# Performance work log

Hardware: AMD Instinct MI355X
Metric: run time of the kernel (lower is better)

## Reference

```python
import jax, jax.numpy as jnp
import numpy as np

RES = 128            # occupancy grid resolution per axis
HIDDEN = 128         # MLP width
PE_POS = 10          # positional-encoding freqs for xyz
PE_DIR = 4           # positional-encoding freqs for viewdirs
S_MAX = 192          # max marching steps per ray
STEP = 0.027         # render_step_size (~aabb diagonal / S_MAX)
ERT = 1e-4           # early_stop_eps (transmittance threshold)
AABB_MIN = -1.5
AABB_MAX = 1.5
WHITE_BKGD = 1.0     # white_bkgd=True


def _posenc(x, L):
    # x: [..., 3] -> [..., 3 + 6L]
    freqs = 2.0 ** jnp.arange(L, dtype=x.dtype)
    xb = x[..., None, :] * freqs[:, None]                 # [..., L, 3]
    enc = jnp.concatenate([jnp.sin(xb), jnp.cos(xb)], axis=-1)  # [..., L, 6]
    return jnp.concatenate([x, enc.reshape(x.shape[:-1] + (-1,))], axis=-1)


def setup_inputs() -> dict:
    key = jax.random.key(0)
    ks = jax.random.split(key, 8)
    B, N = 1, 2048
    # camera origins on a sphere of radius 2.5 outside the aabb, rays aimed near the center
    o = jax.random.normal(ks[0], (B, N, 3), dtype=jnp.float32)
    o = o / jnp.linalg.norm(o, axis=-1, keepdims=True) * 2.5
    target = jax.random.normal(ks[1], (B, N, 3), dtype=jnp.float32) * 0.3
    d = target - o
    d = d / jnp.linalg.norm(d, axis=-1, keepdims=True)
    occ_grid = jax.random.bernoulli(ks[2], 0.3, (RES, RES, RES))
    din_pos = 3 + 6 * PE_POS   # 63
    din_dir = 3 + 6 * PE_DIR   # 27
    sc = lambda n: 1.0 / np.sqrt(n)
    W0 = jax.random.normal(ks[3], (din_pos, HIDDEN), dtype=jnp.float32) * sc(din_pos)
    W1 = jax.random.normal(ks[4], (HIDDEN, HIDDEN), dtype=jnp.float32) * sc(HIDDEN)
    w_sigma = jax.random.normal(ks[5], (HIDDEN, 1), dtype=jnp.float32) * sc(HIDDEN)
    W2 = jax.random.normal(ks[6], (HIDDEN + din_dir, HIDDEN), dtype=jnp.float32) * sc(HIDDEN)
    w_rgb = jax.random.normal(ks[7], (HIDDEN, 3), dtype=jnp.float32) * sc(HIDDEN)
    return {"rays_o": o, "viewdirs": d, "occ_grid": occ_grid,
            "W0": W0, "W1": W1, "w_sigma": w_sigma, "W2": W2, "w_rgb": w_rgb}


def reference(rays_o, viewdirs, occ_grid, W0, W1, w_sigma, W2, w_rgb):
    B, N, _ = rays_o.shape
    o = rays_o.reshape(-1, 3)          # [R, 3]
    d = viewdirs.reshape(-1, 3)        # [R, 3]
    R = o.shape[0]
    # ray / aabb intersection
    inv_d = 1.0 / jnp.where(jnp.abs(d) < 1e-9, 1e-9, d)
    t0 = (AABB_MIN - o) * inv_d
    t1 = (AABB_MAX - o) * inv_d
    t_near = jnp.maximum(jnp.max(jnp.minimum(t0, t1), axis=-1), 0.0)  # [R]
    t_far = jnp.min(jnp.maximum(t0, t1), axis=-1)                     # [R]
    # fixed-step marching (padded to S_MAX, masked) == nerfacc sampling with occ grid
    i = jnp.arange(S_MAX, dtype=rays_o.dtype)
    t_start = t_near[:, None] + STEP * i[None, :]   # [R, S]
    t_end = t_start + STEP
    t_mid = t_start + 0.5 * STEP
    inside = (t_mid < t_far[:, None]) & ((t_far > t_near)[:, None])
    pts = o[:, None, :] + d[:, None, :] * t_mid[..., None]  # [R, S, 3]
    # occupancy lookup (skip empty cells)
    gidx = jnp.clip(((pts - AABB_MIN) / (AABB_MAX - AABB_MIN) * RES).astype(jnp.int32), 0, RES - 1)
    occ = occ_grid[gidx[..., 0], gidx[..., 1], gidx[..., 2]]  # [R, S] bool
    mask = inside & occ
    # NeRF MLP (rgb_alpha_fn): sigma from pos, rgb from pos feature + viewdir
    pe_p = _posenc(pts.reshape(-1, 3), PE_POS)                               # [RS, 63]
    pe_d = _posenc(jnp.broadcast_to(d[:, None, :], pts.shape).reshape(-1, 3), PE_DIR)  # [RS, 27]
    h = jax.nn.relu(pe_p @ W0)
    h = jax.nn.relu(h @ W1)
    sigma = (h @ w_sigma).reshape(R, S_MAX)
    h2 = jax.nn.relu(jnp.concatenate([h, pe_d], axis=-1) @ W2)
    rgb = jax.nn.sigmoid(h2 @ w_rgb).reshape(R, S_MAX, 3)
    # alpha compositing (nerfacc.rendering) with early termination
    delta = t_end - t_start
    alpha = (1.0 - jnp.exp(-jax.nn.relu(sigma) * delta)) * mask.astype(sigma.dtype)
    trans = jnp.cumprod(1.0 - alpha + 1e-10, axis=-1)
    T = jnp.concatenate([jnp.ones((R, 1), alpha.dtype), trans[:, :-1]], axis=-1)  # exclusive
    T = T * (T > ERT).astype(T.dtype)  # early ray termination
    w = T * alpha                      # [R, S]
    rgb_map = jnp.einsum('rs,rsc->rc', w, rgb)
    opacity = jnp.sum(w, axis=-1, keepdims=True)
    depth = jnp.sum(w * t_mid, axis=-1, keepdims=True)
    rgb_map = rgb_map + (1.0 - opacity) * WHITE_BKGD
    return (rgb_map.reshape(B, N, 3), depth.reshape(B, N, 1), opacity.reshape(B, N, 1))
```

## Files before the change

kernel.cpp:

```cpp
#include <hip/hip_runtime.h>
#include <stdint.h>

#define NRAYS 2048
#define SMAX  192
#define RESG  128
#define STEPF 0.027f
#define ERTF  1e-4f
#define CAP   (NRAYS * SMAX)

typedef __attribute__((ext_vector_type(8)))  short bf16x8;
typedef __attribute__((ext_vector_type(16))) float f32x16;

__device__ __forceinline__ uint32_t f2b(float x) {
    uint32_t u = __builtin_bit_cast(uint32_t, x);
    return (u + 0x7fffu + ((u >> 16) & 1u)) >> 16;
}
__device__ __forceinline__ uint32_t bpack(float lo, float hi) {
    return f2b(lo) | (f2b(hi) << 16);
}

__device__ __forceinline__ void ray_aabb(float ox, float oy, float oz,
                                         float dx, float dy, float dz,
                                         float& tn, float& tf) {
    float ix = 1.0f / ((fabsf(dx) < 1e-9f) ? 1e-9f : dx);
    float iy = 1.0f / ((fabsf(dy) < 1e-9f) ? 1e-9f : dy);
    float iz = 1.0f / ((fabsf(dz) < 1e-9f) ? 1e-9f : dz);
    float t0x = (-1.5f - ox) * ix, t1x = (1.5f - ox) * ix;
    float t0y = (-1.5f - oy) * iy, t1y = (1.5f - oy) * iy;
    float t0z = (-1.5f - oz) * iz, t1z = (1.5f - oz) * iz;
    float tnx = fminf(t0x, t1x), tfx = fmaxf(t0x, t1x);
    float tny = fminf(t0y, t1y), tfy = fmaxf(t0y, t1y);
    float tnz = fminf(t0z, t1z), tfz = fmaxf(t0z, t1z);
    tn = fmaxf(fmaxf(fmaxf(tnx, tny), tnz), 0.0f);
    tf = fminf(fminf(tfx, tfy), tfz);
}

__global__ __launch_bounds__(256) void k_count_prep(
        const float* __restrict__ ro, const float* __restrict__ rd,
        const int* __restrict__ occ,
        const float* __restrict__ W0, const float* __restrict__ W1,
        const float* __restrict__ W2,
        int* __restrict__ rayCount, unsigned long long* __restrict__ masks,
        uint32_t* __restrict__ wfrag) {
    int b = blockIdx.x;
    if (b >= NRAYS / 4) {
        int pb = b - NRAYS / 4;
        int lane = threadIdx.x;
        if (lane >= 64) return;
        int g = pb >> 2, oc = pb & 3;
        int out = oc * 32 + (lane & 31);
        const float* W; int kbase, Klim;
        if (g < 4)       { W = W0; kbase = g * 16;        Klim = 63;  }
        else if (g < 12) { W = W1; kbase = (g - 4) * 16;  Klim = 128; }
        else             { W = W2; kbase = (g - 12) * 16; Klim = 155; }
        uint32_t d[4];
        #pragma unroll
        for (int h = 0; h < 4; ++h) {
            int k0 = kbase + ((lane >> 5) << 3) + h * 2;
            float lo = (k0     < Klim) ? W[(size_t)k0 * 128 + out]       : 0.0f;
            float hi = (k0 + 1 < Klim) ? W[(size_t)(k0 + 1) * 128 + out] : 0.0f;
            d[h] = bpack(lo, hi);
        }
        ((uint4*)wfrag)[pb * 64 + lane] = make_uint4(d[0], d[1], d[2], d[3]);
        return;
    }
    int r = b * 4 + (threadIdx.x >> 6);
    int lane = threadIdx.x & 63;
    float ox = ro[r*3+0], oy = ro[r*3+1], oz = ro[r*3+2];
    float dx = rd[r*3+0], dy = rd[r*3+1], dz = rd[r*3+2];
    float tn, tf;
    ray_aabb(ox, oy, oz, dx, dy, dz, tn, tf);
    int cnt = 0;
    #pragma unroll
    for (int c = 0; c < 3; ++c) {
        int s = c * 64 + lane;
        float t_mid = (tn + STEPF * (float)s) + 0.5f * STEPF;
        bool inside = (t_mid < tf) && (tf > tn);
        bool act = false;
        if (inside) {
            float px = ox + dx * t_mid;
            float py = oy + dy * t_mid;
            float pz = oz + dz * t_mid;
            int gx = min(max((int)((px + 1.5f) / 3.0f * 128.0f), 0), RESG - 1);
            int gy = min(max((int)((py + 1.5f) / 3.0f * 128.0f), 0), RESG - 1);
            int gz = min(max((int)((pz + 1.5f) / 3.0f * 128.0f), 0), RESG - 1);
            act = occ[(gx * RESG + gy) * RESG + gz] != 0;
        }
        unsigned long long mb = __ballot(act);
        if (lane == 0) masks[r * 3 + c] = mb;
        cnt += __popcll(mb);
    }
    if (lane == 0) rayCount[r] = cnt;
}

__global__ __launch_bounds__(1024) void k_scan(
        const int* __restrict__ rayCount, int* __restrict__ rayOff,
        int* __restrict__ cnt_total) {
    __shared__ int wsum[16];
    int tid = threadIdx.x;
    int a = rayCount[2 * tid], b = rayCount[2 * tid + 1];
    int s = a + b;
    int lane = tid & 63, w = tid >> 6;
    int v = s;
    #pragma unroll
    for (int off = 1; off < 64; off <<= 1) {
        int t = __shfl_up(v, off);
        if (lane >= off) v += t;
    }
    if (lane == 63) wsum[w] = v;
    __syncthreads();
    if (tid < 16) {
        int x = wsum[tid];
        #pragma unroll
        for (int off = 1; off < 16; off <<= 1) {
            int t = __shfl_up(x, off, 16);
            if (tid >= off) x += t;
        }
        wsum[tid] = x;
    }
    __syncthreads();
    int wbase = (w == 0) ? 0 : wsum[w - 1];
    int incl = wbase + v;
    int excl = incl - s;
    rayOff[2 * tid]     = excl;
    rayOff[2 * tid + 1] = excl + a;
    if (tid == 1023) cnt_total[0] = incl;
}

__global__ __launch_bounds__(256) void k_fill(
        const float* __restrict__ ro, const float* __restrict__ rd,
        const int* __restrict__ rayOff, const unsigned long long* __restrict__ masks,
        int* __restrict__ rayid, float4* __restrict__ pos) {
    int r = blockIdx.x * 4 + (threadIdx.x >> 6);
    int lane = threadIdx.x & 63;
    float ox = ro[r*3+0], oy = ro[r*3+1], oz = ro[r*3+2];
    float dx = rd[r*3+0], dy = rd[r*3+1], dz = rd[r*3+2];
    float tn, tf;
    ray_aabb(ox, oy, oz, dx, dy, dz, tn, tf);
    int base = rayOff[r];
    #pragma unroll
    for (int c = 0; c < 3; ++c) {
        unsigned long long m = masks[r * 3 + c];
        if ((m >> lane) & 1ull) {
            int within = __popcll(m & ((1ull << lane) - 1ull));
            int s = c * 64 + lane;
            float t_mid = (tn + STEPF * (float)s) + 0.5f * STEPF;
            float px = ox + dx * t_mid;
            float py = oy + dy * t_mid;
            float pz = oz + dz * t_mid;
            rayid[base + within] = r;
            pos[base + within] = make_float4(px, py, pz, t_mid);
        }
        base += __popcll(m);
    }
}

__global__ __launch_bounds__(512) void k_mlp(
        const uint32_t* __restrict__ wfrag, const float* __restrict__ wsig,
        const float* __restrict__ wrgb, const float* __restrict__ vd,
        const int* __restrict__ cnt, const int* __restrict__ rayid,
        const float4* __restrict__ pos, float4* __restrict__ rgba) {
    __shared__ __align__(16) short actA[128 * 128];
    __shared__ __align__(16) short bufB[128 * 256];
    __shared__ float4 sPos[128];
    __shared__ int    sRay[128];
    __shared__ float  sV[128];
    __shared__ float  sR[384];

    const int tid  = threadIdx.x;
    const int wave = tid >> 6;
    const int lane = tid & 63;
    const int oc   = wave & 3;
    const int sc   = wave >> 2;
    const int lo5  = lane & 31;
    const int hi5  = lane >> 5;

    if (tid < 128) sV[tid] = wsig[tid];
    if (tid >= 128 && tid < 512) sR[tid - 128] = wrgb[tid - 128];

    bf16x8 wf[22];
    {
        const uint4* src = (const uint4*)wfrag;
        #pragma unroll
        for (int g = 0; g < 22; ++g) {
            uint4 v = src[(g * 4 + oc) * 64 + lane];
            wf[g] = __builtin_bit_cast(bf16x8, v);
        }
    }

    const int total  = *cnt;
    const int ntiles = (total + 127) >> 7;
    const int mrow   = sc * 64 + lo5;
    const int rswz   = (mrow & 15) << 4;

    for (int t = blockIdx.x; t < ntiles; t += gridDim.x) {
        const int base = t << 7;
        __syncthreads();
        if (tid < 128) {
            int gi = base + tid;
            if (gi < total) { sRay[tid] = rayid[gi]; sPos[tid] = pos[gi]; }
            else            { sRay[tid] = 0; sPos[tid] = make_float4(0.f,0.f,0.f,0.f); }
        }
        __syncthreads();

        {
            int m = tid >> 2, p = tid & 3;
            float4 P = sPos[m];
            int swz = (m & 15) << 4;
            #pragma unroll
            for (int half = 0; half < 2; ++half) {
                uint32_t dw[4];
                #pragma unroll
                for (int jp = 0; jp < 4; ++jp) {
                    float v[2];
                    #pragma unroll
                    for (int q = 0; q < 2; ++q) {
                        int c = p * 16 + half * 8 + jp * 2 + q;
                        float val;
                        if (c < 3)        val = (c == 0) ? P.x : ((c == 1) ? P.y : P.z);
                        else if (c >= 63) val = 0.0f;
                        else {
                            int cc = c - 3, l = cc / 6, jj = cc - 6 * l;
                            int a3 = (jj >= 3) ? jj - 3 : jj;
                            float comp = (a3 == 0) ? P.x : ((a3 == 1) ? P.y : P.z);
                            float arg = comp * (float)(1 << l);
                            val = (jj < 3) ? __sinf(arg) : __cosf(arg);
                        }
                        v[q] = val;
                    }
                    dw[jp] = bpack(v[0], v[1]);
                }
                *(uint4*)((char*)actA + m * 256 + ((p * 32 + half * 16) ^ swz)) = make_uint4(dw[0], dw[1], dw[2], dw[3]);
            }
            {
                int ray = sRay[m];
                float Dx = vd[ray*3+0], Dy = vd[ray*3+1], Dz = vd[ray*3+2];
                uint32_t dw[4];
                #pragma unroll
                for (int jp = 0; jp < 4; ++jp) {
                    float v[2];
                    #pragma unroll
                    for (int q = 0; q < 2; ++q) {
                        int c = p * 8 + jp * 2 + q;
                        float val;
                        if (c < 3)        val = (c == 0) ? Dx : ((c == 1) ? Dy : Dz);
                        else if (c >= 27) val = 0.0f;
                        else {
                            int cc = c - 3, l = cc / 6, jj = cc - 6 * l;
                            int a3 = (jj >= 3) ? jj - 3 : jj;
                            float comp = (a3 == 0) ? Dx : ((a3 == 1) ? Dy : Dz);
                            float arg = comp * (float)(1 << l);
                            val = (jj < 3) ? __sinf(arg) : __cosf(arg);
                        }
                        v[q] = val;
                    }
                    dw[jp] = bpack(v[0], v[1]);
                }
                *(uint4*)((char*)bufB + m * 512 + ((256 + p * 16) ^ swz)) = make_uint4(dw[0], dw[1], dw[2], dw[3]);
            }
        }
        __syncthreads();

        {
            f32x16 a0 = {}, a1 = {};
            #pragma unroll
            for (int kb = 0; kb < 4; ++kb) {
                int cb = (kb * 32 + (hi5 << 4)) ^ rswz;
                bf16x8 b0 = *(const bf16x8*)((const char*)actA + mrow * 256 + cb);
                bf16x8 b1 = *(const bf16x8*)((const char*)actA + (mrow + 32) * 256 + cb);
                a0 = __builtin_amdgcn_mfma_f32_32x32x16_bf16(wf[kb], b0, a0, 0, 0, 0);
                a1 = __builtin_amdgcn_mfma_f32_32x32x16_bf16(wf[kb], b1, a1, 0, 0, 0);
            }
            #pragma unroll
            for (int g = 0; g < 4; ++g) {
                int outb = (oc * 32 + g * 8 + (hi5 << 2)) * 2;
                *(uint2*)((char*)bufB + mrow * 512 + (outb ^ rswz)) =
                    make_uint2(bpack(fmaxf(a0[g*4+0],0.f), fmaxf(a0[g*4+1],0.f)),
                               bpack(fmaxf(a0[g*4+2],0.f), fmaxf(a0[g*4+3],0.f)));
                *(uint2*)((char*)bufB + (mrow + 32) * 512 + (outb ^ rswz)) =
                    make_uint2(bpack(fmaxf(a1[g*4+0],0.f), fmaxf(a1[g*4+1],0.f)),
                               bpack(fmaxf(a1[g*4+2],0.f), fmaxf(a1[g*4+3],0.f)));
            }
        }
        __syncthreads();

        {
            f32x16 a0 = {}, a1 = {};
            #pragma unroll
            for (int kb = 0; kb < 8; ++kb) {
                int cb = (kb * 32 + (hi5 << 4)) ^ rswz;
                bf16x8 b0 = *(const bf16x8*)((const char*)bufB + mrow * 512 + cb);
                bf16x8 b1 = *(const bf16x8*)((const char*)bufB + (mrow + 32) * 512 + cb);
                a0 = __builtin_amdgcn_mfma_f32_32x32x16_bf16(wf[4 + kb], b0, a0, 0, 0, 0);
                a1 = __builtin_amdgcn_mfma_f32_32x32x16_bf16(wf[4 + kb], b1, a1, 0, 0, 0);
            }
            #pragma unroll
            for (int g = 0; g < 4; ++g) {
                int outb = (oc * 32 + g * 8 + (hi5 << 2)) * 2;
                *(uint2*)((char*)actA + mrow * 256 + (outb ^ rswz)) =
                    make_uint2(bpack(fmaxf(a0[g*4+0],0.f), fmaxf(a0[g*4+1],0.f)),
                               bpack(fmaxf(a0[g*4+2],0.f), fmaxf(a0[g*4+3],0.f)));
                *(uint2*)((char*)actA + (mrow + 32) * 256 + (outb ^ rswz)) =
                    make_uint2(bpack(fmaxf(a1[g*4+0],0.f), fmaxf(a1[g*4+1],0.f)),
                               bpack(fmaxf(a1[g*4+2],0.f), fmaxf(a1[g*4+3],0.f)));
            }
        }
        __syncthreads();

        {
            f32x16 a0 = {}, a1 = {};
            #pragma unroll
            for (int kb = 0; kb < 8; ++kb) {
                int cb = (kb * 32 + (hi5 << 4)) ^ rswz;
                bf16x8 b0 = *(const bf16x8*)((const char*)actA + mrow * 256 + cb);
                bf16x8 b1 = *(const bf16x8*)((const char*)actA + (mrow + 32) * 256 + cb);
                a0 = __builtin_amdgcn_mfma_f32_32x32x16_bf16(wf[12 + kb], b0, a0, 0, 0, 0);
                a1 = __builtin_amdgcn_mfma_f32_32x32x16_bf16(wf[12 + kb], b1, a1, 0, 0, 0);
            }
            #pragma unroll
            for (int kb = 8; kb < 10; ++kb) {
                int cb = (kb * 32 + (hi5 << 4)) ^ rswz;
                bf16x8 b0 = *(const bf16x8*)((const char*)bufB + mrow * 512 + cb);
                bf16x8 b1 = *(const bf16x8*)((const char*)bufB + (mrow + 32) * 512 + cb);
                a0 = __builtin_amdgcn_mfma_f32_32x32x16_bf16(wf[12 + kb], b0, a0, 0, 0, 0);
                a1 = __builtin_amdgcn_mfma_f32_32x32x16_bf16(wf[12 + kb], b1, a1, 0, 0, 0);
            }
            #pragma unroll
            for (int g = 0; g < 4; ++g) {
                int outb = (oc * 32 + g * 8 + (hi5 << 2)) * 2;
                *(uint2*)((char*)bufB + mrow * 512 + (outb ^ rswz)) =
                    make_uint2(bpack(fmaxf(a0[g*4+0],0.f), fmaxf(a0[g*4+1],0.f)),
                               bpack(fmaxf(a0[g*4+2],0.f), fmaxf(a0[g*4+3],0.f)));
                *(uint2*)((char*)bufB + (mrow + 32) * 512 + (outb ^ rswz)) =
                    make_uint2(bpack(fmaxf(a1[g*4+0],0.f), fmaxf(a1[g*4+1],0.f)),
                               bpack(fmaxf(a1[g*4+2],0.f), fmaxf(a1[g*4+3],0.f)));
            }
        }
        __syncthreads();

        {
            int m = tid >> 2, p = tid & 3;
            int swz = (m & 15) << 4;
            float sp = 0.f, r0 = 0.f, r1 = 0.f, r2 = 0.f;
            #pragma unroll
            for (int hh = 0; hh < 4; ++hh) {
                uint4 q = *(const uint4*)((const char*)actA + m * 256 + ((p * 64 + hh * 16) ^ swz));
                uint32_t w[4] = {q.x, q.y, q.z, q.w};
                #pragma unroll
                for (int e = 0; e < 4; ++e) {
                    int j = p * 32 + hh * 8 + e * 2;
                    float a0 = __builtin_bit_cast(float, w[e] << 16);
                    float a1 = __builtin_bit_cast(float, w[e] & 0xffff0000u);
                    sp = fmaf(a0, sV[j], sp);
                    sp = fmaf(a1, sV[j + 1], sp);
                }
            }
            #pragma unroll
            for (int hh = 0; hh < 4; ++hh) {
                uint4 q = *(const uint4*)((const char*)bufB + m * 512 + ((p * 64 + hh * 16) ^ swz));
                uint32_t w[4] = {q.x, q.y, q.z, q.w};
                #pragma unroll
                for (int e = 0; e < 4; ++e) {
                    int j = p * 32 + hh * 8 + e * 2;
                    float a0 = __builtin_bit_cast(float, w[e] << 16);
                    float a1 = __builtin_bit_cast(float, w[e] & 0xffff0000u);
                    r0 = fmaf(a0, sR[j*3+0], r0); r1 = fmaf(a0, sR[j*3+1], r1); r2 = fmaf(a0, sR[j*3+2], r2);
                    r0 = fmaf(a1, sR[(j+1)*3+0], r0); r1 = fmaf(a1, sR[(j+1)*3+1], r1); r2 = fmaf(a1, sR[(j+1)*3+2], r2);
                }
            }
            #pragma unroll
            for (int off = 1; off < 4; off <<= 1) {
                sp += __shfl_xor(sp, off);
                r0 += __shfl_xor(r0, off);
                r1 += __shfl_xor(r1, off);
                r2 += __shfl_xor(r2, off);
            }
            if (p == 0 && (base + m) < total) {
                float alpha = 1.0f - __expf(-fmaxf(sp, 0.0f) * STEPF);
                float c0 = 1.0f / (1.0f + __expf(-r0));
                float c1 = 1.0f / (1.0f + __expf(-r1));
                float c2 = 1.0f / (1.0f + __expf(-r2));
                rgba[base + m] = make_float4(c0, c1, c2, alpha);
            }
        }
    }
}

__global__ __launch_bounds__(256) void k_render(
        const int* __restrict__ rayOff, const int* __restrict__ rayCount,
        const float4* __restrict__ rgba, const float* __restrict__ posw,
        float* __restrict__ out) {
    int r = blockIdx.x * 4 + (threadIdx.x >> 6);
    int lane = threadIdx.x & 63;
    int off = rayOff[r], cnt = rayCount[r];
    float T_run = 1.0f;
    float cr = 0.f, cg = 0.f, cb = 0.f, opa = 0.f, dep = 0.f;
    for (int j = 0; j < cnt; j += 64) {
        int idx = j + lane;
        float4 f = make_float4(0.f, 0.f, 0.f, 0.f);
        float tmid = 0.f;
        if (idx < cnt) {
            f = rgba[off + idx];
            tmid = posw[(size_t)(off + idx) * 4 + 3];
        }
        float p = (1.0f - f.w) + 1e-10f;
        #pragma unroll
        for (int o = 1; o < 64; o <<= 1) {
            float v = __shfl_up(p, o);
            if (lane >= o) p *= v;
        }
        float pprev = __shfl_up(p, 1);
        float Texc = (lane == 0) ? T_run : T_run * pprev;
        Texc = (Texc > ERTF) ? Texc : 0.0f;
        float w = Texc * f.w;
        cr += w * f.x; cg += w * f.y; cb += w * f.z;
        opa += w; dep += w * tmid;
        T_run *= __shfl(p, 63);
        if (T_run <= ERTF) break;
    }
    #pragma unroll
    for (int o = 32; o; o >>= 1) {
        cr  += __shfl_xor(cr, o);
        cg  += __shfl_xor(cg, o);
        cb  += __shfl_xor(cb, o);
        opa += __shfl_xor(opa, o);
        dep += __shfl_xor(dep, o);
    }
    if (lane == 0) {
        out[r * 3 + 0] = cr + (1.0f - opa);
        out[r * 3 + 1] = cg + (1.0f - opa);
        out[r * 3 + 2] = cb + (1.0f - opa);
        out[NRAYS * 3 + r] = dep;
        out[NRAYS * 4 + r] = opa;
    }
}

extern "C" void kernel_launch(void* const* d_in, const int* in_sizes, int n_in,
                              void* d_out, int out_size, void* d_ws, size_t ws_size,
                              hipStream_t stream) {
    const float* ro   = (const float*)d_in[0];
    const float* rd   = (const float*)d_in[1];
    const int*   occ  = (const int*)d_in[2];
    const float* W0   = (const float*)d_in[3];
    const float* W1   = (const float*)d_in[4];
    const float* wsig = (const float*)d_in[5];
    const float* W2   = (const float*)d_in[6];
    const float* wrgb = (const float*)d_in[7];
    float* out = (float*)d_out;

    char* ws = (char*)d_ws;
    int*                cnt_total = (int*)ws;
    int*                rayCount  = (int*)(ws + 16);
    int*                rayOff    = (int*)(ws + 8208);
    unsigned long long* masks     = (unsigned long long*)(ws + 16400);
    int*                rayid     = (int*)(ws + 65552);
    float4*             pos       = (float4*)(ws + 65552 + (size_t)CAP * 8);
    float4*             rgba      = (float4*)(ws + 65552 + (size_t)CAP * 24);
    uint32_t*           wfrag     = (uint32_t*)(ws + 65552 + (size_t)CAP * 40);

    k_count_prep <<<NRAYS / 4 + 88, 256, 0, stream>>>(ro, rd, occ, W0, W1, W2,
                                                      rayCount, masks, wfrag);
    k_scan  <<<1, 1024, 0, stream>>>(rayCount, rayOff, cnt_total);
    k_fill  <<<NRAYS / 4, 256, 0, stream>>>(ro, rd, rayOff, masks, rayid, pos);
    k_mlp   <<<256, 512, 0, stream>>>(wfrag, wsig, wrgb, rd, cnt_total, rayid, pos, rgba);
    k_render<<<NRAYS / 4, 256, 0, stream>>>(rayOff, rayCount, rgba, (const float*)pos, out);
}
```

Measured before the change: 114.2 us.

## Fuse count, scan, fill, MLP and render into one per-8-ray kernel

New measurement: 115.6 us. Within noise of the previous version (+1.2%).

```diff
diff --git a/kernel.cpp b/kernel.cpp
--- a/kernel.cpp
+++ b/kernel.cpp
@@ -6,7 +6,6 @@
 #define RESG  128
 #define STEPF 0.027f
 #define ERTF  1e-4f
-#define CAP   (NRAYS * SMAX)
 
 typedef __attribute__((ext_vector_type(8)))  short bf16x8;
 typedef __attribute__((ext_vector_type(16))) float f32x16;
@@ -35,42 +34,62 @@
     tf = fminf(fminf(tfx, tfy), tfz);
 }
 
-__global__ __launch_bounds__(256) void k_count_prep(
+__global__ __launch_bounds__(512) void k_fused(
         const float* __restrict__ ro, const float* __restrict__ rd,
         const int* __restrict__ occ,
         const float* __restrict__ W0, const float* __restrict__ W1,
-        const float* __restrict__ W2,
-        int* __restrict__ rayCount, unsigned long long* __restrict__ masks,
-        uint32_t* __restrict__ wfrag) {
-    int b = blockIdx.x;
-    if (b >= NRAYS / 4) {
-        int pb = b - NRAYS / 4;
-        int lane = threadIdx.x;
-        if (lane >= 64) return;
-        int g = pb >> 2, oc = pb & 3;
-        int out = oc * 32 + (lane & 31);
-        const float* W; int kbase, Klim;
-        if (g < 4)       { W = W0; kbase = g * 16;        Klim = 63;  }
-        else if (g < 12) { W = W1; kbase = (g - 4) * 16;  Klim = 128; }
-        else             { W = W2; kbase = (g - 12) * 16; Klim = 155; }
-        uint32_t d[4];
+        const float* __restrict__ wsig, const float* __restrict__ W2,
+        const float* __restrict__ wrgb, float* __restrict__ out) {
+    __shared__ __align__(16) short actA[128 * 128];
+    __shared__ __align__(16) short bufB[128 * 256];
+    __shared__ float4 rgbaL[8 * SMAX];
+    __shared__ unsigned short sList[8 * SMAX];
+    __shared__ float  sPD[8][28];
+    __shared__ float  sRD[8][8];
+    __shared__ float  sV[128];
+    __shared__ float  sR[384];
+    __shared__ int    sCnt[8];
+
+    const int tid  = threadIdx.x;
+    const int wave = tid >> 6;
+    const int lane = tid & 63;
+    const int oc   = wave & 3;
+    const int sc   = wave >> 2;
+    const int lo5  = lane & 31;
+    const int hi5  = lane >> 5;
+
+    if (tid < 128) sV[tid] = wsig[tid];
+    if (tid >= 128 && tid < 512) sR[tid - 128] = wrgb[tid - 128];
+
+    bf16x8 wf[22];
+    {
+        const int outc = oc * 32 + lo5;
         #pragma unroll
-        for (int h = 0; h < 4; ++h) {
-            int k0 = kbase + ((lane >> 5) << 3) + h * 2;
-            float lo = (k0     < Klim) ? W[(size_t)k0 * 128 + out]       : 0.0f;
-            float hi = (k0 + 1 < Klim) ? W[(size_t)(k0 + 1) * 128 + out] : 0.0f;
-            d[h] = bpack(lo, hi);
-        }
-        ((uint4*)wfrag)[pb * 64 + lane] = make_uint4(d[0], d[1], d[2], d[3]);
-        return;
-    }
-    int r = b * 4 + (threadIdx.x >> 6);
-    int lane = threadIdx.x & 63;
-    float ox = ro[r*3+0], oy = ro[r*3+1], oz = ro[r*3+2];
-    float dx = rd[r*3+0], dy = rd[r*3+1], dz = rd[r*3+2];
+        for (int g = 0; g < 22; ++g) {
+            const float* W; int kbase, Klim;
+            if (g < 4)       { W = W0; kbase = g * 16;        Klim = 63;  }
+            else if (g < 12) { W = W1; kbase = (g - 4) * 16;  Klim = 128; }
+            else             { W = W2; kbase = (g - 12) * 16; Klim = 155; }
+            uint32_t d[4];
+            #pragma unroll
+            for (int h = 0; h < 4; ++h) {
+                int k0 = kbase + (hi5 << 3) + h * 2;
+                float lo = (k0     < Klim) ? W[(size_t)k0 * 128 + outc]       : 0.0f;
+                float hi = (k0 + 1 < Klim) ? W[(size_t)(k0 + 1) * 128 + outc] : 0.0f;
+                d[h] = bpack(lo, hi);
+            }
+            uint4 v = make_uint4(d[0], d[1], d[2], d[3]);
+            wf[g] = __builtin_bit_cast(bf16x8, v);
+        }
+    }
+
+    const int r = blockIdx.x * 8 + wave;
+    const float ox = ro[r*3+0], oy = ro[r*3+1], oz = ro[r*3+2];
+    const float dx = rd[r*3+0], dy = rd[r*3+1], dz = rd[r*3+2];
     float tn, tf;
     ray_aabb(ox, oy, oz, dx, dy, dz, tn, tf);
-    int cnt = 0;
+    unsigned long long msk[3];
+    int myCnt = 0;
     #pragma unroll
     for (int c = 0; c < 3; ++c) {
         int s = c * 64 + lane;
@@ -87,125 +106,73 @@
             act = occ[(gx * RESG + gy) * RESG + gz] != 0;
         }
         unsigned long long mb = __ballot(act);
-        if (lane == 0) masks[r * 3 + c] = mb;
-        cnt += __popcll(mb);
-    }
-    if (lane == 0) rayCount[r] = cnt;
-}
-
-__global__ __launch_bounds__(1024) void k_scan(
-        const int* __restrict__ rayCount, int* __restrict__ rayOff,
-        int* __restrict__ cnt_total) {
-    __shared__ int wsum[16];
-    int tid = threadIdx.x;
-    int a = rayCount[2 * tid], b = rayCount[2 * tid + 1];
-    int s = a + b;
-    int lane = tid & 63, w = tid >> 6;
-    int v = s;
+        msk[c] = mb;
+        myCnt += __popcll(mb);
+    }
+    if (lane == 0) {
+        sCnt[wave] = myCnt;
+        sRD[wave][0] = ox; sRD[wave][1] = oy; sRD[wave][2] = oz;
+        sRD[wave][3] = dx; sRD[wave][4] = dy; sRD[wave][5] = dz;
+        sRD[wave][6] = tn;
+    }
+    if (lane < 28) {
+        float val = 0.0f;
+        if (lane < 3) val = (lane == 0) ? dx : ((lane == 1) ? dy : dz);
+        else if (lane < 27) {
+            int cc = lane - 3, l = cc / 6, jj = cc - 6 * l;
+            int a3 = (jj >= 3) ? jj - 3 : jj;
+            float comp = (a3 == 0) ? dx : ((a3 == 1) ? dy : dz);
+            float arg = comp * (float)(1 << l);
+            val = (jj < 3) ? __sinf(arg) : __cosf(arg);
+        }
+        sPD[wave][lane] = val;
+    }
+    __syncthreads();
+
+    int myBase = 0, total = 0;
     #pragma unroll
-    for (int off = 1; off < 64; off <<= 1) {
-        int t = __shfl_up(v, off);
-        if (lane >= off) v += t;
-    }
-    if (lane == 63) wsum[w] = v;
+    for (int i = 0; i < 8; ++i) {
+        int ci = sCnt[i];
+        if (i < wave) myBase += ci;
+        total += ci;
+    }
+    {
+        int run = myBase;
+        #pragma unroll
+        for (int c = 0; c < 3; ++c) {
+            unsigned long long mb = msk[c];
+            if ((mb >> lane) & 1ull) {
+                int within = __popcll(mb & ((1ull << lane) - 1ull));
+                sList[run + within] = (unsigned short)((wave << 8) | (c * 64 + lane));
+            }
+            run += __popcll(mb);
+        }
+    }
     __syncthreads();
-    if (tid < 16) {
-        int x = wsum[tid];
-        #pragma unroll
-        for (int off = 1; off < 16; off <<= 1) {
-            int t = __shfl_up(x, off, 16);
-            if (tid >= off) x += t;
-        }
-        wsum[tid] = x;
-    }
-    __syncthreads();
-    int wbase = (w == 0) ? 0 : wsum[w - 1];
-    int incl = wbase + v;
-    int excl = incl - s;
-    rayOff[2 * tid]     = excl;
-    rayOff[2 * tid + 1] = excl + a;
-    if (tid == 1023) cnt_total[0] = incl;
-}
-
-__global__ __launch_bounds__(256) void k_fill(
-        const float* __restrict__ ro, const float* __restrict__ rd,
-        const int* __restrict__ rayOff, const unsigned long long* __restrict__ masks,
-        int* __restrict__ rayid, float4* __restrict__ pos) {
-    int r = blockIdx.x * 4 + (threadIdx.x >> 6);
-    int lane = threadIdx.x & 63;
-    float ox = ro[r*3+0], oy = ro[r*3+1], oz = ro[r*3+2];
-    float dx = rd[r*3+0], dy = rd[r*3+1], dz = rd[r*3+2];
-    float tn, tf;
-    ray_aabb(ox, oy, oz, dx, dy, dz, tn, tf);
-    int base = rayOff[r];
-    #pragma unroll
-    for (int c = 0; c < 3; ++c) {
-        unsigned long long m = masks[r * 3 + c];
-        if ((m >> lane) & 1ull) {
-            int within = __popcll(m & ((1ull << lane) - 1ull));
-            int s = c * 64 + lane;
-            float t_mid = (tn + STEPF * (float)s) + 0.5f * STEPF;
-            float px = ox + dx * t_mid;
-            float py = oy + dy * t_mid;
-            float pz = oz + dz * t_mid;
-            rayid[base + within] = r;
-            pos[base + within] = make_float4(px, py, pz, t_mid);
-        }
-        base += __popcll(m);
-    }
-}
-
-__global__ __launch_bounds__(512) void k_mlp(
-        const uint32_t* __restrict__ wfrag, const float* __restrict__ wsig,
-        const float* __restrict__ wrgb, const float* __restrict__ vd,
-        const int* __restrict__ cnt, const int* __restrict__ rayid,
-        const float4* __restrict__ pos, float4* __restrict__ rgba) {
-    __shared__ __align__(16) short actA[128 * 128];
-    __shared__ __align__(16) short bufB[128 * 256];
-    __shared__ float4 sPos[128];
-    __shared__ int    sRay[128];
-    __shared__ float  sV[128];
-    __shared__ float  sR[384];
-
-    const int tid  = threadIdx.x;
-    const int wave = tid >> 6;
-    const int lane = tid & 63;
-    const int oc   = wave & 3;
-    const int sc   = wave >> 2;
-    const int lo5  = lane & 31;
-    const int hi5  = lane >> 5;
-
-    if (tid < 128) sV[tid] = wsig[tid];
-    if (tid >= 128 && tid < 512) sR[tid - 128] = wrgb[tid - 128];
-
-    bf16x8 wf[22];
-    {
-        const uint4* src = (const uint4*)wfrag;
-        #pragma unroll
-        for (int g = 0; g < 22; ++g) {
-            uint4 v = src[(g * 4 + oc) * 64 + lane];
-            wf[g] = __builtin_bit_cast(bf16x8, v);
-        }
-    }
-
-    const int total  = *cnt;
+
     const int ntiles = (total + 127) >> 7;
     const int mrow   = sc * 64 + lo5;
     const int rswz   = (mrow & 15) << 4;
 
-    for (int t = blockIdx.x; t < ntiles; t += gridDim.x) {
+    for (int t = 0; t < ntiles; ++t) {
         const int base = t << 7;
         __syncthreads();
-        if (tid < 128) {
-            int gi = base + tid;
-            if (gi < total) { sRay[tid] = rayid[gi]; sPos[tid] = pos[gi]; }
-            else            { sRay[tid] = 0; sPos[tid] = make_float4(0.f,0.f,0.f,0.f); }
-        }
-        __syncthreads();
 
         {
             int m = tid >> 2, p = tid & 3;
-            float4 P = sPos[m];
+            int gi = base + m;
+            float px = 0.f, py = 0.f, pz = 0.f;
+            int we = 0;
+            if (gi < total) {
+                int e = sList[gi];
+                we = e >> 8;
+                int s = e & 255;
+                float tnw = sRD[we][6];
+                float t_mid = (tnw + STEPF * (float)s) + 0.5f * STEPF;
+                px = sRD[we][0] + sRD[we][3] * t_mid;
+                py = sRD[we][1] + sRD[we][4] * t_mid;
+                pz = sRD[we][2] + sRD[we][5] * t_mid;
+            }
             int swz = (m & 15) << 4;
             #pragma unroll
             for (int half = 0; half < 2; ++half) {
@@ -217,12 +184,12 @@
                     for (int q = 0; q < 2; ++q) {
                         int c = p * 16 + half * 8 + jp * 2 + q;
                         float val;
-                        if (c < 3)        val = (c == 0) ? P.x : ((c == 1) ? P.y : P.z);
+                        if (c < 3)        val = (c == 0) ? px : ((c == 1) ? py : pz);
                         else if (c >= 63) val = 0.0f;
                         else {
                             int cc = c - 3, l = cc / 6, jj = cc - 6 * l;
                             int a3 = (jj >= 3) ? jj - 3 : jj;
-                            float comp = (a3 == 0) ? P.x : ((a3 == 1) ? P.y : P.z);
+                            float comp = (a3 == 0) ? px : ((a3 == 1) ? py : pz);
                             float arg = comp * (float)(1 << l);
                             val = (jj < 3) ? __sinf(arg) : __cosf(arg);
                         }
@@ -233,8 +200,6 @@
                 *(uint4*)((char*)actA + m * 256 + ((p * 32 + half * 16) ^ swz)) = make_uint4(dw[0], dw[1], dw[2], dw[3]);
             }
             {
-                int ray = sRay[m];
-                float Dx = vd[ray*3+0], Dy = vd[ray*3+1], Dz = vd[ray*3+2];
                 uint32_t dw[4];
                 #pragma unroll
                 for (int jp = 0; jp < 4; ++jp) {
@@ -242,17 +207,7 @@
                     #pragma unroll
                     for (int q = 0; q < 2; ++q) {
                         int c = p * 8 + jp * 2 + q;
-                        float val;
-                        if (c < 3)        val = (c == 0) ? Dx : ((c == 1) ? Dy : Dz);
-                        else if (c >= 27) val = 0.0f;
-                        else {
-                            int cc = c - 3, l = cc / 6, jj = cc - 6 * l;
-                            int a3 = (jj >= 3) ? jj - 3 : jj;
-                            float comp = (a3 == 0) ? Dx : ((a3 == 1) ? Dy : Dz);
-                            float arg = comp * (float)(1 << l);
-                            val = (jj < 3) ? __sinf(arg) : __cosf(arg);
-                        }
-                        v[q] = val;
+                        v[q] = (c < 28) ? sPD[we][c] : 0.0f;
                     }
                     dw[jp] = bpack(v[0], v[1]);
                 }
@@ -340,6 +295,7 @@
 
         {
             int m = tid >> 2, p = tid & 3;
+            int gi = base + m;
             int swz = (m & 15) << 4;
             float sp = 0.f, r0 = 0.f, r1 = 0.f, r2 = 0.f;
             #pragma unroll
@@ -375,63 +331,59 @@
                 r1 += __shfl_xor(r1, off);
                 r2 += __shfl_xor(r2, off);
             }
-            if (p == 0 && (base + m) < total) {
+            if (p == 0 && gi < total) {
                 float alpha = 1.0f - __expf(-fmaxf(sp, 0.0f) * STEPF);
                 float c0 = 1.0f / (1.0f + __expf(-r0));
                 float c1 = 1.0f / (1.0f + __expf(-r1));
                 float c2 = 1.0f / (1.0f + __expf(-r2));
-                rgba[base + m] = make_float4(c0, c1, c2, alpha);
-            }
-        }
-    }
-}
-
-__global__ __launch_bounds__(256) void k_render(
-        const int* __restrict__ rayOff, const int* __restrict__ rayCount,
-        const float4* __restrict__ rgba, const float* __restrict__ posw,
-        float* __restrict__ out) {
-    int r = blockIdx.x * 4 + (threadIdx.x >> 6);
-    int lane = threadIdx.x & 63;
-    int off = rayOff[r], cnt = rayCount[r];
-    float T_run = 1.0f;
-    float cr = 0.f, cg = 0.f, cb = 0.f, opa = 0.f, dep = 0.f;
-    for (int j = 0; j < cnt; j += 64) {
-        int idx = j + lane;
-        float4 f = make_float4(0.f, 0.f, 0.f, 0.f);
-        float tmid = 0.f;
-        if (idx < cnt) {
-            f = rgba[off + idx];
-            tmid = posw[(size_t)(off + idx) * 4 + 3];
-        }
-        float p = (1.0f - f.w) + 1e-10f;
+                rgbaL[gi] = make_float4(c0, c1, c2, alpha);
+            }
+        }
+    }
+    __syncthreads();
+
+    {
+        float T_run = 1.0f;
+        float cr = 0.f, cg = 0.f, cb = 0.f, opa = 0.f, dep = 0.f;
+        for (int j = 0; j < myCnt; j += 64) {
+            int idx = j + lane;
+            float4 f = make_float4(0.f, 0.f, 0.f, 0.f);
+            float tmid = 0.f;
+            if (idx < myCnt) {
+                f = rgbaL[myBase + idx];
+                int s = sList[myBase + idx] & 255;
+                tmid = (tn + STEPF * (float)s) + 0.5f * STEPF;
+            }
+            float p = (1.0f - f.w) + 1e-10f;
+            #pragma unroll
+            for (int o = 1; o < 64; o <<= 1) {
+                float v = __shfl_up(p, o);
+                if (lane >= o) p *= v;
+            }
+            float pprev = __shfl_up(p, 1);
+            float Texc = (lane == 0) ? T_run : T_run * pprev;
+            Texc = (Texc > ERTF) ? Texc : 0.0f;
+            float w = Texc * f.w;
+            cr += w * f.x; cg += w * f.y; cb += w * f.z;
+            opa += w; dep += w * tmid;
+            T_run *= __shfl(p, 63);
+            if (T_run <= ERTF) break;
+        }
         #pragma unroll
-        for (int o = 1; o < 64; o <<= 1) {
-            float v = __shfl_up(p, o);
-            if (lane >= o) p *= v;
-        }
-        float pprev = __shfl_up(p, 1);
-        float Texc = (lane == 0) ? T_run : T_run * pprev;
-        Texc = (Texc > ERTF) ? Texc : 0.0f;
-        float w = Texc * f.w;
-        cr += w * f.x; cg += w * f.y; cb += w * f.z;
-        opa += w; dep += w * tmid;
-        T_run *= __shfl(p, 63);
-        if (T_run <= ERTF) break;
-    }
-    #pragma unroll
-    for (int o = 32; o; o >>= 1) {
-        cr  += __shfl_xor(cr, o);
-        cg  += __shfl_xor(cg, o);
-        cb  += __shfl_xor(cb, o);
-        opa += __shfl_xor(opa, o);
-        dep += __shfl_xor(dep, o);
-    }
-    if (lane == 0) {
-        out[r * 3 + 0] = cr + (1.0f - opa);
-        out[r * 3 + 1] = cg + (1.0f - opa);
-        out[r * 3 + 2] = cb + (1.0f - opa);
-        out[NRAYS * 3 + r] = dep;
-        out[NRAYS * 4 + r] = opa;
+        for (int o = 32; o; o >>= 1) {
+            cr  += __shfl_xor(cr, o);
+            cg  += __shfl_xor(cg, o);
+            cb  += __shfl_xor(cb, o);
+            opa += __shfl_xor(opa, o);
+            dep += __shfl_xor(dep, o);
+        }
+        if (lane == 0) {
+            out[r * 3 + 0] = cr + (1.0f - opa);
+            out[r * 3 + 1] = cg + (1.0f - opa);
+            out[r * 3 + 2] = cb + (1.0f - opa);
+            out[NRAYS * 3 + r] = dep;
+            out[NRAYS * 4 + r] = opa;
+        }
     }
 }
 
@@ -448,20 +400,5 @@
     const float* wrgb = (const float*)d_in[7];
     float* out = (float*)d_out;
 
-    char* ws = (char*)d_ws;
-    int*                cnt_total = (int*)ws;
-    int*                rayCount  = (int*)(ws + 16);
-    int*                rayOff    = (int*)(ws + 8208);
-    unsigned long long* masks     = (unsigned long long*)(ws + 16400);
-    int*                rayid     = (int*)(ws + 65552);
-    float4*             pos       = (float4*)(ws + 65552 + (size_t)CAP * 8);
-    float4*             rgba      = (float4*)(ws + 65552 + (size_t)CAP * 24);
-    uint32_t*           wfrag     = (uint32_t*)(ws + 65552 + (size_t)CAP * 40);
-
-    k_count_prep <<<NRAYS / 4 + 88, 256, 0, stream>>>(ro, rd, occ, W0, W1, W2,
-                                                      rayCount, masks, wfrag);
-    k_scan  <<<1, 1024, 0, stream>>>(rayCount, rayOff, cnt_total);
-    k_fill  <<<NRAYS / 4, 256, 0, stream>>>(ro, rd, rayOff, masks, rayid, pos);
-    k_mlp   <<<256, 512, 0, stream>>>(wfrag, wsig, wrgb, rd, cnt_total, rayid, pos, rgba);
-    k_render<<<NRAYS / 4, 256, 0, stream>>>(rayOff, rayCount, rgba, (const float*)pos, out);
+    k_fused<<<NRAYS / 8, 512, 0, stream>>>(ro, rd, occ, W0, W1, wsig, W2, wrgb, out);
 }
```
